# Performance work log

Measured on AMD Instinct MI355X. Metric: run time of the kernel, lower is better.

Reference implementation:

```python
import jax, jax.numpy as jnp
import numpy as np
import math

B, N, D_MODEL, H, D_HEAD = 2, 2048, 1024, 16, 64
EPS = 1e-6

def setup_inputs() -> dict:
    key = jax.random.key(0)
    ks = jax.random.split(key, 6)
    s = 1.0 / math.sqrt(D_MODEL)
    return {
        "X": jax.random.normal(ks[0], (B, N, D_MODEL), dtype=jnp.float32),
        "Wq": jax.random.normal(ks[1], (D_MODEL, H * D_HEAD), dtype=jnp.float32) * s,
        "Wk": jax.random.normal(ks[2], (D_MODEL, H * D_HEAD), dtype=jnp.float32) * s,
        "Wv": jax.random.normal(ks[3], (D_MODEL, H * D_HEAD), dtype=jnp.float32) * s,
        "Wo": jax.random.normal(ks[4], (H * D_HEAD, D_MODEL), dtype=jnp.float32) * s,
        "bo": jnp.zeros((D_MODEL,), dtype=jnp.float32),
    }

def reference(X, Wq, Wk, Wv, Wo, bo):
    b, n, _ = X.shape
    # project and split heads -> [b, h, n, d_head]
    def heads(Y):
        return Y.reshape(b, n, H, D_HEAD).transpose(0, 2, 1, 3)
    Q = heads(X @ Wq)
    K = heads(X @ Wk)
    V = heads(X @ Wv)
    # per-head L2 normalization of Q and K
    Q = Q / (jnp.linalg.norm(Q, axis=-1, keepdims=True) + EPS)
    K = K / (jnp.linalg.norm(K, axis=-1, keepdims=True) + EPS)
    # scores [b, h, n, n]
    A = jnp.einsum("bhqd,bhkd->bhqk", Q, K) / math.sqrt(D_HEAD)
    causal = jnp.triu(jnp.ones((n, n), dtype=bool), k=1)
    A = jnp.where(causal, -jnp.inf, A)
    A = jax.nn.softmax(A, axis=-1)
    V_hat = jnp.einsum("bhqk,bhkd->bhqd", A, V)
    V_hat = V_hat.transpose(0, 2, 1, 3).reshape(b, n, H * D_HEAD)
    return V_hat @ Wo + bo
```

## Files before the change

### kernel.cpp

```cpp
#include <hip/hip_runtime.h>
#include <hip/hip_bf16.h>
#include <math.h>

#define BATCH 2
#define NSEQ  2048
#define DM    1024
#define NH    16
#define DH    64
#define EPS_N 1e-6f

typedef unsigned short u16;
typedef __attribute__((ext_vector_type(8))) short short8;
typedef __attribute__((ext_vector_type(8))) unsigned short u16x8;
typedef __attribute__((ext_vector_type(4))) unsigned short u16x4;
typedef __attribute__((ext_vector_type(4))) float f32x4;

__device__ __forceinline__ u16 f2bf(float x) {
  __hip_bfloat16 h = __float2bfloat16(x);
  return *reinterpret_cast<u16*>(&h);
}

__device__ __forceinline__ void gl_lds16(const u16* g, u16* lds_base) {
  __builtin_amdgcn_global_load_lds(
      (__attribute__((address_space(1))) void*)g,
      (__attribute__((address_space(3))) void*)lds_base, 16, 0, 0);
}

__global__ __launch_bounds__(256) void prep(
    const float* __restrict__ X,
    const float* __restrict__ w0, const float* __restrict__ w1,
    const float* __restrict__ w2, const float* __restrict__ w3,
    u16* __restrict__ Xb, u16* __restrict__ WT) {
  const int id = blockIdx.x, tid = threadIdx.x;
  if (id >= 1024) {
    size_t base = ((size_t)(id - 1024) * 256 + tid) * 8;
    float4 f0 = *(const float4*)&X[base];
    float4 f1 = *(const float4*)&X[base + 4];
    u16x8 v;
    v[0] = f2bf(f0.x); v[1] = f2bf(f0.y); v[2] = f2bf(f0.z); v[3] = f2bf(f0.w);
    v[4] = f2bf(f1.x); v[5] = f2bf(f1.y); v[6] = f2bf(f1.z); v[7] = f2bf(f1.w);
    *(u16x8*)&Xb[base] = v;
    return;
  }
  const int z = id >> 8, xy = id & 255, bx = xy & 15, by = xy >> 4;
  const float* in = (z == 0) ? w0 : (z == 1) ? w1 : (z == 2) ? w2 : w3;
  u16* o = WT + (size_t)z * DM * DM;
  __shared__ u16 T[64][65];
  const int n0 = bx * 64, k0 = by * 64;
  #pragma unroll
  for (int i = 0; i < 4; i++) {
    int c = tid + 256 * i, row = c >> 4, col4 = c & 15;
    float4 f = *(const float4*)&in[(size_t)(k0 + row) * DM + n0 + col4 * 4];
    T[row][col4 * 4 + 0] = f2bf(f.x);
    T[row][col4 * 4 + 1] = f2bf(f.y);
    T[row][col4 * 4 + 2] = f2bf(f.z);
    T[row][col4 * 4 + 3] = f2bf(f.w);
  }
  __syncthreads();
  #pragma unroll
  for (int i = 0; i < 2; i++) {
    int c = tid + 256 * i, row = c >> 3, col8 = c & 7;
    u16x8 v;
    #pragma unroll
    for (int e = 0; e < 8; e++) v[e] = T[col8 * 8 + e][row];
    *(u16x8*)&o[(size_t)(n0 + row) * DM + k0 + col8 * 8] = v;
  }
}

#define GEMM_STAGE(Aptr, Btptr, koff, buf)                                     \
  do {                                                                         \
    _Pragma("unroll") for (int L = 0; L < 2; L++) {                            \
      int I = w * 2 + L;                                    \
      gl_lds16(Aptr + (size_t)(m0 + I * 8 + srow) * DM + (koff) + scol,        \
               As[buf] + I * 512);                                             \
    }                                                                          \
    _Pragma("unroll") for (int L = 0; L < 4; L++) {                            \
      int I = w * 4 + L;                                   \
      gl_lds16(Btptr + (size_t)(n0 + I * 8 + srow) * DM + (koff) + scol,       \
               Bs[buf] + I * 512);                                             \
    }                                                                          \
  } while (0)

#define GEMM64x128_MAINLOOP(Aptr, Btptr)                                       \
  __shared__ u16 As[2][64 * 64];                                               \
  __shared__ u16 Bs[2][128 * 64];                                              \
  const int tid = threadIdx.x, w = tid >> 6, lane = tid & 63;                  \
  const int ml = lane & 15, quad = lane >> 4;                                  \
  const int m0 = blockIdx.y * 64, n0 = blockIdx.x * 128;                       \
  const int wm = w & 1, wn = w >> 1;                                           \
  const int srow = lane >> 3;                      \
  const int scol = ((lane & 7) ^ srow) * 8;         \
  f32x4 acc[2][4];                                                             \
  _Pragma("unroll") for (int mi = 0; mi < 2; mi++)                             \
    _Pragma("unroll") for (int ni = 0; ni < 4; ni++)                           \
      _Pragma("unroll") for (int e = 0; e < 4; e++) acc[mi][ni][e] = 0.f;      \
  GEMM_STAGE(Aptr, Btptr, 0, 0);                                               \
  __syncthreads();                               \
  int cur = 0;                                                                 \
  for (int k0 = 0; k0 < DM; k0 += 64) {                                        \
    if (k0 + 64 < DM) GEMM_STAGE(Aptr, Btptr, k0 + 64, cur ^ 1);               \
    _Pragma("unroll") for (int kk = 0; kk < 64; kk += 32) {                    \
      const int kc = kk >> 3;                          \
      short8 am[2], bn[4];                                                     \
      _Pragma("unroll") for (int i = 0; i < 2; i++) {                          \
        int ra = wm * 32 + i * 16 + ml;                                        \
        am[i] = *(const short8*)&As[cur][ra * 64 +                             \
                                         (((quad + kc) ^ (ra & 7)) * 8)];      \
      }                                                                        \
      _Pragma("unroll") for (int i = 0; i < 4; i++) {                          \
        int rb = wn * 64 + i * 16 + ml;                                        \
        bn[i] = *(const short8*)&Bs[cur][rb * 64 +                             \
                                         (((quad + kc) ^ (rb & 7)) * 8)];      \
      }                                                                        \
      _Pragma("unroll") for (int mi = 0; mi < 2; mi++)                         \
        _Pragma("unroll") for (int ni = 0; ni < 4; ni++)                       \
          acc[mi][ni] = __builtin_amdgcn_mfma_f32_16x16x32_bf16(               \
              am[mi], bn[ni], acc[mi][ni], 0, 0, 0);                           \
    }                                                                          \
    __syncthreads();           \
    cur ^= 1;                                                                  \
  }

__global__ __launch_bounds__(256) void gemm_qkv128(
    const u16* __restrict__ Xb, const u16* __restrict__ WT,
    u16* __restrict__ Qo, u16* __restrict__ Ko, u16* __restrict__ Vt) {
  const u16* Bt = WT + (size_t)blockIdx.z * DM * DM;
  GEMM64x128_MAINLOOP(Xb, Bt)
  const int z = blockIdx.z;
  if (z < 2) {
    u16* OutQK = (z == 0) ? Qo : Ko;
    const float qsc = (z == 0) ? 0.125f : 1.0f;
    const int h = (n0 >> 6) + wn;
    #pragma unroll
    for (int mi = 0; mi < 2; mi++) {
      int mrow0 = m0 + wm * 32 + mi * 16 + quad * 4;
      int b = mrow0 >> 11, tok0 = mrow0 & (NSEQ - 1);
      #pragma unroll
      for (int r = 0; r < 4; r++) {
        float ss = 0.f;
        #pragma unroll
        for (int ni = 0; ni < 4; ni++) ss += acc[mi][ni][r] * acc[mi][ni][r];
        ss += __shfl_xor(ss, 1, 64);
        ss += __shfl_xor(ss, 2, 64);
        ss += __shfl_xor(ss, 4, 64);
        ss += __shfl_xor(ss, 8, 64);
        float sc = qsc / (sqrtf(ss) + EPS_N);
        #pragma unroll
        for (int ni = 0; ni < 4; ni++)
          OutQK[((size_t)(b * NH + h) * NSEQ + tok0 + r) * DH + ni * 16 + ml] =
              f2bf(acc[mi][ni][r] * sc);
      }
    }
  } else {
    #pragma unroll
    for (int mi = 0; mi < 2; mi++) {
      int mrow0 = m0 + wm * 32 + mi * 16 + quad * 4;
      int b = mrow0 >> 11, tok0 = mrow0 & (NSEQ - 1);
      #pragma unroll
      for (int ni = 0; ni < 4; ni++) {
        int n = n0 + wn * 64 + ni * 16 + ml;
        int h = n >> 6, d = n & 63;
        u16x4 pk;
        #pragma unroll
        for (int r = 0; r < 4; r++) pk[r] = f2bf(acc[mi][ni][r]);
        *(u16x4*)&Vt[((size_t)(b * NH + h) * DH + d) * NSEQ + tok0] = pk;
      }
    }
  }
}

__global__ __launch_bounds__(256) void gemm_proj128(
    const u16* __restrict__ A, const u16* __restrict__ BtW,
    const float* __restrict__ bias, float* __restrict__ out) {
  GEMM64x128_MAINLOOP(A, BtW)
  #pragma unroll
  for (int ni = 0; ni < 4; ni++) {
    int n = n0 + wn * 64 + ni * 16 + ml;
    float bz = bias[n];
    #pragma unroll
    for (int mi = 0; mi < 2; mi++) {
      int mrow0 = m0 + wm * 32 + mi * 16 + quad * 4;
      #pragma unroll
      for (int r = 0; r < 4; r++)
        out[(size_t)(mrow0 + r) * DM + n] = acc[mi][ni][r] + bz;
    }
  }
}

__global__ __launch_bounds__(512) void flash_attn(
    const u16* __restrict__ Qb, const u16* __restrict__ Kb,
    const u16* __restrict__ Vt, u16* __restrict__ vhat) {
  const int tid = threadIdx.x, w = tid >> 6, lane = tid & 63;
  const int ml = lane & 15, quad = lane >> 4;
  const int wq = w & 3, wk = w >> 2;
  const int bh = blockIdx.x;
  const int bb = bh >> 4, hb = bh & 15;
  const int pairY = blockIdx.y;
  const u16* Qh = Qb + (size_t)bh * NSEQ * DH;
  const u16* Kh = Kb + (size_t)bh * NSEQ * DH;
  const u16* Vth = Vt + (size_t)bh * DH * NSEQ;

  __shared__ u16 Ks [64 * 64];
  __shared__ u16 VsT[64 * 64];
  __shared__ u16 Ps [8][16][40];
  __shared__ float Os[4][16][66];
  __shared__ float Ls[4][16];

  const int srow8 = lane >> 3;
  const int sch   = lane & 7;
  const int sslot = sch ^ srow8;

  for (int ph = 0; ph < 2; ph++) {
    const int qb64 = ph ? (31 - pairY) : pairY;
    const int q0 = qb64 * 64;
    const int ntiles = qb64 + 1;

    short8 aq[2];
    #pragma unroll
    for (int c = 0; c < 2; c++)
      aq[c] = *(const short8*)&Qh[(size_t)(q0 + wq * 16 + ml) * DH + c * 32 + quad * 8];

    f32x4 oacc[4];
    #pragma unroll
    for (int n = 0; n < 4; n++)
      #pragma unroll
      for (int e = 0; e < 4; e++) oacc[n][e] = 0.f;
    float l_[4] = {0.f, 0.f, 0.f, 0.f};

    u16x8 kreg, vreg;
    kreg = *(const u16x8*)&Kh[(size_t)(w * 8 + srow8) * DH + sch * 8];
    vreg = *(const u16x8*)&Vth[(size_t)(w * 8 + srow8) * NSEQ + sch * 8];

    for (int t = 0; t < ntiles; t++) {
      const int j0 = t * 64;
      __syncthreads();
      *(u16x8*)&Ks [(w * 8 + srow8) * 64 + sslot * 8] = kreg;
      *(u16x8*)&VsT[(w * 8 + srow8) * 64 + sslot * 8] = vreg;
      __syncthreads();

      if (t + 1 < ntiles) {
        const int j1 = j0 + 64;
        kreg = *(const u16x8*)&Kh[(size_t)(j1 + w * 8 + srow8) * DH + sch * 8];
        vreg = *(const u16x8*)&Vth[(size_t)(w * 8 + srow8) * NSEQ + j1 + sch * 8];
      }

      f32x4 sacc[2];
      #pragma unroll
      for (int n = 0; n < 2; n++)
        #pragma unroll
        for (int e = 0; e < 4; e++) sacc[n][e] = 0.f;
      #pragma unroll
      for (int c = 0; c < 2; c++)
        #pragma unroll
        for (int n = 0; n < 2; n++) {
          int kr = wk * 32 + n * 16 + ml;
          short8 bf = *(const short8*)&Ks[kr * 64 + (((c * 4 + quad) ^ (kr & 7)) * 8)];
          sacc[n] = __builtin_amdgcn_mfma_f32_16x16x32_bf16(aq[c], bf, sacc[n], 0, 0, 0);
        }

      const bool lastt = (t == ntiles - 1);
      float p[2][4];
      #pragma unroll
      for (int n = 0; n < 2; n++) {
        int j = j0 + wk * 32 + n * 16 + ml;
        #pragma unroll
        for (int r = 0; r < 4; r++) {
          int q = q0 + wq * 16 + quad * 4 + r;
          float e = __expf(sacc[n][r]);
          p[n][r] = (lastt && j > q) ? 0.f : e;
          l_[r] += p[n][r];
        }
      }

      #pragma unroll
      for (int n = 0; n < 2; n++)
        #pragma unroll
        for (int r = 0; r < 4; r++)
          Ps[w][quad * 4 + r][n * 16 + ml] = f2bf(p[n][r]);

      short8 ap = *(const short8*)&Ps[w][ml][quad * 8];
      #pragma unroll
      for (int n = 0; n < 4; n++) {
        int dr = n * 16 + ml;
        short8 bv = *(const short8*)&VsT[dr * 64 + (((wk * 4 + quad) ^ (dr & 7)) * 8)];
        oacc[n] = __builtin_amdgcn_mfma_f32_16x16x32_bf16(ap, bv, oacc[n], 0, 0, 0);
      }
    }

    float lred[4];
    #pragma unroll
    for (int r = 0; r < 4; r++) {
      float lv = l_[r];
      lv += __shfl_xor(lv, 1, 64);
      lv += __shfl_xor(lv, 2, 64);
      lv += __shfl_xor(lv, 4, 64);
      lv += __shfl_xor(lv, 8, 64);
      lred[r] = lv;
    }
    if (wk == 0) {
      #pragma unroll
      for (int n = 0; n < 4; n++)
        #pragma unroll
        for (int r = 0; r < 4; r++)
          Os[wq][quad * 4 + r][n * 16 + ml] = oacc[n][r];
      if (ml == 0) {
        #pragma unroll
        for (int r = 0; r < 4; r++) Ls[wq][quad * 4 + r] = lred[r];
      }
    }
    __syncthreads();
    if (wk == 1) {
      #pragma unroll
      for (int r = 0; r < 4; r++) {
        float inv = 1.f / (lred[r] + Ls[wq][quad * 4 + r]);
        int q = q0 + wq * 16 + quad * 4 + r;
        #pragma unroll
        for (int n = 0; n < 4; n++) {
          float o = oacc[n][r] + Os[wq][quad * 4 + r][n * 16 + ml];
          vhat[((size_t)(bb * NSEQ + q)) * DM + hb * DH + n * 16 + ml] =
              f2bf(o * inv);
        }
      }
    }
    __syncthreads();
  }
}

extern "C" void kernel_launch(void* const* d_in, const int* in_sizes, int n_in,
                              void* d_out, int out_size, void* d_ws, size_t ws_size,
                              hipStream_t stream) {
  const float* X  = (const float*)d_in[0];
  const float* Wq = (const float*)d_in[1];
  const float* Wk = (const float*)d_in[2];
  const float* Wv = (const float*)d_in[3];
  const float* Wo = (const float*)d_in[4];
  const float* bo = (const float*)d_in[5];
  float* out = (float*)d_out;

  const size_t NE = (size_t)BATCH * NSEQ * DM;
  u16* Qb   = (u16*)d_ws;
  u16* Kb   = Qb + NE;
  u16* Vt   = Kb + NE;
  u16* XbVh = Vt + NE;
  u16* WT   = XbVh + NE;

  prep        <<<dim3(3072),      256, 0, stream>>>(X, Wq, Wk, Wv, Wo, XbVh, WT);
  gemm_qkv128 <<<dim3(8, 64, 3),  256, 0, stream>>>(XbVh, WT, Qb, Kb, Vt);
  flash_attn  <<<dim3(32, 16),    512, 0, stream>>>(Qb, Kb, Vt, XbVh);
  gemm_proj128<<<dim3(8, 64, 1),  256, 0, stream>>>(XbVh, WT + 3 * (size_t)DM * DM,
                                                    bo, out);
}
```

Baseline: 187.0 us.

## Process 128-key tiles per iteration in causal flash attention

Doubles the K/V tile per loop iteration from 64 to 128 keys, so each wave handles 64 keys and issues twice as many MFMAs between barriers. This halves the number of syncthreads and global prefetch rounds per query block. In exchange it uses more LDS and registers, and because the tile count is now (qb64/2)+1, some query blocks compute an extra fully masked half-tile of work.

```diff
diff --git a/kernel.cpp b/kernel.cpp
--- a/kernel.cpp
+++ b/kernel.cpp
@@ -200,9 +200,9 @@
   const u16* Kh = Kb + (size_t)bh * NSEQ * DH;
   const u16* Vth = Vt + (size_t)bh * DH * NSEQ;
 
-  __shared__ u16 Ks [64 * 64];
-  __shared__ u16 VsT[64 * 64];
-  __shared__ u16 Ps [8][16][40];
+  __shared__ u16 Ks [128 * 64];
+  __shared__ u16 VsT[64 * 128];
+  __shared__ u16 Ps [8][16][72];
   __shared__ float Os[4][16][66];
   __shared__ float Ls[4][16];
 
@@ -213,7 +213,7 @@
   for (int ph = 0; ph < 2; ph++) {
     const int qb64 = ph ? (31 - pairY) : pairY;
     const int q0 = qb64 * 64;
-    const int ntiles = qb64 + 1;
+    const int ntiles = (qb64 >> 1) + 1;
 
     short8 aq[2];
     #pragma unroll
@@ -227,42 +227,51 @@
       for (int e = 0; e < 4; e++) oacc[n][e] = 0.f;
     float l_[4] = {0.f, 0.f, 0.f, 0.f};
 
-    u16x8 kreg, vreg;
-    kreg = *(const u16x8*)&Kh[(size_t)(w * 8 + srow8) * DH + sch * 8];
-    vreg = *(const u16x8*)&Vth[(size_t)(w * 8 + srow8) * NSEQ + sch * 8];
+    u16x8 kreg[2], vreg[2];
+    #pragma unroll
+    for (int i = 0; i < 2; i++) {
+      kreg[i] = *(const u16x8*)&Kh[(size_t)(w * 16 + i * 8 + srow8) * DH + sch * 8];
+      vreg[i] = *(const u16x8*)&Vth[(size_t)(w * 8 + srow8) * NSEQ + (sch + i * 8) * 8];
+    }
 
     for (int t = 0; t < ntiles; t++) {
-      const int j0 = t * 64;
+      const int j0 = t * 128;
       __syncthreads();
-      *(u16x8*)&Ks [(w * 8 + srow8) * 64 + sslot * 8] = kreg;
-      *(u16x8*)&VsT[(w * 8 + srow8) * 64 + sslot * 8] = vreg;
+      #pragma unroll
+      for (int i = 0; i < 2; i++) {
+        *(u16x8*)&Ks [(w * 16 + i * 8 + srow8) * 64 + sslot * 8] = kreg[i];
+        *(u16x8*)&VsT[(w * 8 + srow8) * 128 + (sslot + i * 8) * 8] = vreg[i];
+      }
       __syncthreads();
 
       if (t + 1 < ntiles) {
-        const int j1 = j0 + 64;
-        kreg = *(const u16x8*)&Kh[(size_t)(j1 + w * 8 + srow8) * DH + sch * 8];
-        vreg = *(const u16x8*)&Vth[(size_t)(w * 8 + srow8) * NSEQ + j1 + sch * 8];
-      }
-
-      f32x4 sacc[2];
-      #pragma unroll
-      for (int n = 0; n < 2; n++)
+        const int j1 = j0 + 128;
+        #pragma unroll
+        for (int i = 0; i < 2; i++) {
+          kreg[i] = *(const u16x8*)&Kh[(size_t)(j1 + w * 16 + i * 8 + srow8) * DH + sch * 8];
+          vreg[i] = *(const u16x8*)&Vth[(size_t)(w * 8 + srow8) * NSEQ + j1 + (sch + i * 8) * 8];
+        }
+      }
+
+      f32x4 sacc[4];
+      #pragma unroll
+      for (int n = 0; n < 4; n++)
         #pragma unroll
         for (int e = 0; e < 4; e++) sacc[n][e] = 0.f;
       #pragma unroll
       for (int c = 0; c < 2; c++)
         #pragma unroll
-        for (int n = 0; n < 2; n++) {
-          int kr = wk * 32 + n * 16 + ml;
+        for (int n = 0; n < 4; n++) {
+          int kr = wk * 64 + n * 16 + ml;
           short8 bf = *(const short8*)&Ks[kr * 64 + (((c * 4 + quad) ^ (kr & 7)) * 8)];
           sacc[n] = __builtin_amdgcn_mfma_f32_16x16x32_bf16(aq[c], bf, sacc[n], 0, 0, 0);
         }
 
       const bool lastt = (t == ntiles - 1);
-      float p[2][4];
-      #pragma unroll
-      for (int n = 0; n < 2; n++) {
-        int j = j0 + wk * 32 + n * 16 + ml;
+      float p[4][4];
+      #pragma unroll
+      for (int n = 0; n < 4; n++) {
+        int j = j0 + wk * 64 + n * 16 + ml;
         #pragma unroll
         for (int r = 0; r < 4; r++) {
           int q = q0 + wq * 16 + quad * 4 + r;
@@ -273,17 +282,21 @@
       }
 
       #pragma unroll
-      for (int n = 0; n < 2; n++)
+      for (int n = 0; n < 4; n++)
         #pragma unroll
         for (int r = 0; r < 4; r++)
           Ps[w][quad * 4 + r][n * 16 + ml] = f2bf(p[n][r]);
 
-      short8 ap = *(const short8*)&Ps[w][ml][quad * 8];
-      #pragma unroll
-      for (int n = 0; n < 4; n++) {
-        int dr = n * 16 + ml;
-        short8 bv = *(const short8*)&VsT[dr * 64 + (((wk * 4 + quad) ^ (dr & 7)) * 8)];
-        oacc[n] = __builtin_amdgcn_mfma_f32_16x16x32_bf16(ap, bv, oacc[n], 0, 0, 0);
+      #pragma unroll
+      for (int ks = 0; ks < 2; ks++) {
+        short8 ap = *(const short8*)&Ps[w][ml][ks * 32 + quad * 8];
+        #pragma unroll
+        for (int n = 0; n < 4; n++) {
+          int dr = n * 16 + ml;
+          short8 bv = *(const short8*)&VsT[dr * 128 +
+              ((wk * 8 + ((ks * 4 + quad) ^ (dr & 7))) * 8)];
+          oacc[n] = __builtin_amdgcn_mfma_f32_16x16x32_bf16(ap, bv, oacc[n], 0, 0, 0);
+        }
       }
     }
 
```

Measured after the change: 189.9 us. Within noise of the previous version (+1.6%).
